# Kernel optimization log

Measured on AMD Instinct MI355X. Metric: run time of the kernel, lower is better.

The kernel has to match this reference:

```python
import math
import jax, jax.numpy as jnp
import numpy as np

N_HEAD = 16
N_GROUPS = 32
EPS = 1e-05


def gelu(x):
    return 0.5 * x * (1.0 + jnp.tanh(math.sqrt(2.0 / math.pi) * (x + 0.044715 * x ** 3)))


def dp_group_norm(x, weight, bias, num_groups=N_GROUPS, eps=EPS):
    # x: [B, T, H]. torch F.group_norm on transposed [B, H, T] normalizes over
    # (channels_per_group, T) jointly per (batch, group).
    B, T, H = x.shape
    xg = x.reshape(B, T, num_groups, H // num_groups)
    mean = jnp.mean(xg, axis=(1, 3), keepdims=True)
    var = jnp.mean((xg - mean) ** 2, axis=(1, 3), keepdims=True)
    xn = ((xg - mean) / jnp.sqrt(var + eps)).reshape(B, T, H)
    return xn * weight + bias


def attention(x, w_attn, b_attn, w_aproj, b_aproj):
    B, T, H = x.shape
    hd = H // N_HEAD
    qkv = x @ w_attn + b_attn                      # [B, T, 3H]
    q, k, v = jnp.split(qkv, 3, axis=-1)
    q = q.reshape(B, T, N_HEAD, hd).transpose(0, 2, 1, 3)   # [B, nh, T, hd]
    k = k.reshape(B, T, N_HEAD, hd).transpose(0, 2, 1, 3)   # [B, nh, T, hd]
    v = v.reshape(B, T, N_HEAD, hd).transpose(0, 2, 1, 3)
    w = jnp.einsum('bhqd,bhkd->bhqk', q, k)        # no 1/sqrt(d): scale=False
    causal = jnp.tril(jnp.ones((T, T), dtype=x.dtype))
    w = w * causal - 1e10 * (1.0 - causal)
    w = jax.nn.softmax(w, axis=-1)
    a = jnp.einsum('bhqk,bhkd->bhqd', w, v)        # [B, nh, T, hd]
    a = a.transpose(0, 2, 1, 3).reshape(B, T, H)
    a = a @ w_aproj + b_aproj
    present = jnp.stack((k, v))                    # [2, B, nh, T, hd]
    return a, present


def setup_inputs() -> dict:
    key = jax.random.key(0)
    ks = jax.random.split(key, 6)
    B, T, H = 2, 2048, 1024
    return {
        'x': jax.random.normal(ks[0], (B, T, H), dtype=jnp.float32),
        'w_attn': jax.random.normal(ks[1], (H, 3 * H), dtype=jnp.float32) * 0.02,
        'b_attn': jnp.zeros((3 * H,), dtype=jnp.float32),
        'w_aproj': jax.random.normal(ks[2], (H, H), dtype=jnp.float32) * 0.02,
        'b_aproj': jnp.zeros((H,), dtype=jnp.float32),
        'ln1_w': jnp.ones((H,), dtype=jnp.float32),
        'ln1_b': jnp.zeros((H,), dtype=jnp.float32),
        'ln2_w': jnp.ones((H,), dtype=jnp.float32),
        'ln2_b': jnp.zeros((H,), dtype=jnp.float32),
        'w_fc': jax.random.normal(ks[3], (H, 4 * H), dtype=jnp.float32) * 0.02,
        'b_fc': jnp.zeros((4 * H,), dtype=jnp.float32),
        'w_mproj': jax.random.normal(ks[4], (4 * H, H), dtype=jnp.float32) * 0.02,
        'b_mproj': jnp.zeros((H,), dtype=jnp.float32),
    }


def reference(x, w_attn, b_attn, w_aproj, b_aproj, ln1_w, ln1_b, ln2_w, ln2_b,
              w_fc, b_fc, w_mproj, b_mproj):
    a, present = attention(dp_group_norm(x, ln1_w, ln1_b), w_attn, b_attn, w_aproj, b_aproj)
    x = x + a
    h = gelu(dp_group_norm(x, ln2_w, ln2_b) @ w_fc + b_fc)
    m = h @ w_mproj + b_mproj
    x = x + m
    return (x, present)
```

## Files before the change

### kernel.cpp

```cpp
#include <hip/hip_runtime.h>

#define B_  2
#define T_  2048
#define H_  1024
#define NH_ 16
#define HD_ 64
#define M_  (B_*T_)
#define PS_ 72

typedef __bf16 bf16x8 __attribute__((ext_vector_type(8)));
typedef float  floatx4 __attribute__((ext_vector_type(4)));

typedef __attribute__((address_space(1))) const unsigned int gas_u32;
typedef __attribute__((address_space(3))) unsigned int       las_u32;

__device__ __forceinline__ void gload_lds16(const __bf16* g, __bf16* l) {
    __builtin_amdgcn_global_load_lds((gas_u32*)g, (las_u32*)l, 16, 0, 0);
}

__global__ __launch_bounds__(256) void transpose_bf16(
    const float* __restrict__ in, __bf16* __restrict__ out, int K, int N)
{
    __shared__ float tile[32][33];
    const int k0 = blockIdx.x * 32, n0 = blockIdx.y * 32;
    const int tx = threadIdx.x & 31, ty = threadIdx.x >> 5;
#pragma unroll
    for (int i = 0; i < 32; i += 8)
        tile[ty + i][tx] = in[(size_t)(k0 + ty + i) * N + (n0 + tx)];
    __syncthreads();
#pragma unroll
    for (int i = 0; i < 32; i += 8)
        out[(size_t)(n0 + ty + i) * K + (k0 + tx)] = (__bf16)tile[tx][ty + i];
}

__global__ __launch_bounds__(256) void gn_partial(
    const float* __restrict__ x, float2* __restrict__ part)
{
    const int bg = blockIdx.x, chunk = blockIdx.y;
    const int batch = bg >> 5, g = bg & 31;
    const float* xp = x + (size_t)batch * T_ * H_ + g * 32;
    float s = 0.f, ss = 0.f;
    for (int i = threadIdx.x; i < 128 * 32; i += 256) {
        const int t = chunk * 128 + (i >> 5), c = i & 31;
        const float v = xp[(size_t)t * H_ + c];
        s += v; ss += v * v;
    }
#pragma unroll
    for (int off = 32; off > 0; off >>= 1) {
        s  += __shfl_down(s,  off, 64);
        ss += __shfl_down(ss, off, 64);
    }
    __shared__ float rs[4], rss[4];
    const int wv = threadIdx.x >> 6, lane = threadIdx.x & 63;
    if (lane == 0) { rs[wv] = s; rss[wv] = ss; }
    __syncthreads();
    if (threadIdx.x == 0)
        part[bg * 16 + chunk] =
            make_float2(rs[0] + rs[1] + rs[2] + rs[3],
                        rss[0] + rss[1] + rss[2] + rss[3]);
}

__global__ __launch_bounds__(64) void gn_finalize(
    const float2* __restrict__ part, float2* __restrict__ stats)
{
    const int bg = threadIdx.x;
    float s = 0.f, ss = 0.f;
#pragma unroll
    for (int i = 0; i < 16; ++i) {
        const float2 p = part[bg * 16 + i];
        s += p.x; ss += p.y;
    }
    const float inv = 1.f / (float)(T_ * 32);
    const float mean = s * inv;
    const float var  = ss * inv - mean * mean;
    stats[bg] = make_float2(mean, rsqrtf(var + 1e-5f));
}

__global__ __launch_bounds__(256) void gn_apply(
    const float* __restrict__ x, const float2* __restrict__ stats,
    const float* __restrict__ w, const float* __restrict__ bsc,
    __bf16* __restrict__ out)
{
    const size_t idx = ((size_t)blockIdx.x * 256 + threadIdx.x) * 4;
    const int h = (int)(idx & (H_ - 1));
    const int batch = (int)(idx >> 21);
    const float2 mr = stats[batch * 32 + (h >> 5)];
    const float4 xv = *(const float4*)(x + idx);
    const float4 wv = *(const float4*)(w + h);
    const float4 bv = *(const float4*)(bsc + h);
    __bf16 o[4];
    o[0] = (__bf16)((xv.x - mr.x) * mr.y * wv.x + bv.x);
    o[1] = (__bf16)((xv.y - mr.x) * mr.y * wv.y + bv.y);
    o[2] = (__bf16)((xv.z - mr.x) * mr.y * wv.z + bv.z);
    o[3] = (__bf16)((xv.w - mr.x) * mr.y * wv.w + bv.w);
    *(uint2*)(out + idx) = *(uint2*)o;
}

__device__ __forceinline__ void gemm_core(
    const __bf16* __restrict__ A, const __bf16* __restrict__ BT,
    int K, int m0, int n0, __bf16* As, __bf16* Bs, floatx4 (&acc)[4][4])
{
    const int tid  = threadIdx.x;
    const int lane = tid & 63, wv = tid >> 6;
    const int quad = lane >> 4, l16 = lane & 15;
    const int wm = (wv >> 1) * 64, wn = (wv & 1) * 64;
    const int r0 = tid >> 2;
    const int scs = (((tid & 3) ^ ((r0 >> 1) & 3)) * 8);
    const int xq8 = (quad ^ ((l16 >> 1) & 3)) * 8;

    const __bf16* Ag = A  + (size_t)(m0 + r0) * K + scs;
    const __bf16* Bg = BT + (size_t)(n0 + r0) * K + scs;

#pragma unroll
    for (int s = 0; s < 2; ++s) {
        gload_lds16(Ag + s * 32,                  As + s * 4096 + tid * 8);
        gload_lds16(Ag + (size_t)64 * K + s * 32, As + s * 4096 + 2048 + tid * 8);
        gload_lds16(Bg + s * 32,                  Bs + s * 4096 + tid * 8);
        gload_lds16(Bg + (size_t)64 * K + s * 32, Bs + s * 4096 + 2048 + tid * 8);
    }
    int cur = 0;
    for (int kt = 0; kt < K; kt += 64) {
        if (kt + 64 < K) {
            const int nb = (cur ^ 1) * 8192;
            const int kn = kt + 64;
#pragma unroll
            for (int s = 0; s < 2; ++s) {
                gload_lds16(Ag + kn + s * 32,                  As + nb + s * 4096 + tid * 8);
                gload_lds16(Ag + (size_t)64 * K + kn + s * 32, As + nb + s * 4096 + 2048 + tid * 8);
                gload_lds16(Bg + kn + s * 32,                  Bs + nb + s * 4096 + tid * 8);
                gload_lds16(Bg + (size_t)64 * K + kn + s * 32, Bs + nb + s * 4096 + 2048 + tid * 8);
            }
            asm volatile("s_waitcnt vmcnt(8)" ::: "memory");
        } else {
            asm volatile("s_waitcnt vmcnt(0)" ::: "memory");
        }
        __builtin_amdgcn_s_barrier();
        __builtin_amdgcn_sched_barrier(0);
        const __bf16* Ab = As + cur * 8192;
        const __bf16* Bb = Bs + cur * 8192;
#pragma unroll
        for (int kk = 0; kk < 2; ++kk) {
            bf16x8 af[4], bfg[4];
#pragma unroll
            for (int i = 0; i < 4; ++i)
                af[i]  = *(const bf16x8*)(Ab + kk * 4096 + (wm + i * 16 + l16) * 32 + xq8);
#pragma unroll
            for (int i = 0; i < 4; ++i)
                bfg[i] = *(const bf16x8*)(Bb + kk * 4096 + (wn + i * 16 + l16) * 32 + xq8);
#pragma unroll
            for (int mi = 0; mi < 4; ++mi)
#pragma unroll
                for (int ni = 0; ni < 4; ++ni)
                    acc[mi][ni] = __builtin_amdgcn_mfma_f32_16x16x32_bf16(
                        af[mi], bfg[ni], acc[mi][ni], 0, 0, 0);
        }
        __builtin_amdgcn_sched_barrier(0);
        __builtin_amdgcn_s_barrier();
        __builtin_amdgcn_sched_barrier(0);
        cur ^= 1;
    }
}

#define GEMM_PROLOGUE(KVAL)                                             \
    __shared__ __align__(16) __bf16 As[2 * 8192], Bs[2 * 8192];         \
    const int m0 = blockIdx.x * 128, n0 = blockIdx.y * 128;             \
    floatx4 acc[4][4];                                                  \
    { floatx4 z = {0.f, 0.f, 0.f, 0.f};                                 \
      for (int i = 0; i < 4; ++i) for (int j = 0; j < 4; ++j) acc[i][j] = z; } \
    gemm_core(A, BT, (KVAL), m0, n0, As, Bs, acc);                      \
    const int tid = threadIdx.x, lane = tid & 63, wv = tid >> 6;        \
    const int quad = lane >> 4, l16 = lane & 15;                        \
    const int wm = (wv >> 1) * 64, wn = (wv & 1) * 64;                  \
    (void)tid;

__global__ __launch_bounds__(256) void gemm_qkv(
    const __bf16* __restrict__ A, const __bf16* __restrict__ BT,
    const float* __restrict__ bias, __bf16* __restrict__ qb,
    __bf16* __restrict__ kb, __bf16* __restrict__ vtb,
    float* __restrict__ present)
{
    GEMM_PROLOGUE(H_)
#pragma unroll
    for (int ni = 0; ni < 4; ++ni) {
        const int col = n0 + wn + ni * 16 + l16;
        const float bv = bias[col];
        const int which = col >> 10, c = col & 1023, hh = c >> 6, d = c & 63;
#pragma unroll
        for (int mi = 0; mi < 4; ++mi)
#pragma unroll
            for (int r = 0; r < 4; ++r) {
                const int row = m0 + wm + mi * 16 + quad * 4 + r;
                const int bb = row >> 11, t = row & 2047;
                const float v = acc[mi][ni][r] + bv;
                const size_t idx = (((size_t)bb * NH_ + hh) * T_ + t) * HD_ + d;
                if (which == 0)      qb[idx] = (__bf16)(v * 1.4426950408889634f);
                else if (which == 1) { kb[idx] = (__bf16)v; present[idx] = v; }
                else { vtb[(((size_t)bb * NH_ + hh) * HD_ + d) * T_ + t] = (__bf16)v;
                       present[(size_t)B_ * NH_ * T_ * HD_ + idx] = v; }
            }
    }
}

__global__ __launch_bounds__(256) void gemm_gelu(
    const __bf16* __restrict__ A, const __bf16* __restrict__ BT,
    const float* __restrict__ bias, __bf16* __restrict__ out)
{
    GEMM_PROLOGUE(H_)
#pragma unroll
    for (int ni = 0; ni < 4; ++ni) {
        const int col = n0 + wn + ni * 16 + l16;
        const float bv = bias[col];
#pragma unroll
        for (int mi = 0; mi < 4; ++mi)
#pragma unroll
            for (int r = 0; r < 4; ++r) {
                const int row = m0 + wm + mi * 16 + quad * 4 + r;
                const float v = acc[mi][ni][r] + bv;
                const float e = exp2f(-2.3022082f * (v + 0.044715f * v * v * v));
                float rcp;
                asm("v_rcp_f32 %0, %1" : "=v"(rcp) : "v"(1.f + e));
                out[(size_t)row * (4 * H_) + col] = (__bf16)(v * rcp);
            }
    }
}

__global__ __launch_bounds__(256) void gemm_resid_n64(
    const __bf16* __restrict__ A, const __bf16* __restrict__ BT,
    const float* __restrict__ bias, const float* __restrict__ resid,
    float* __restrict__ out, int K, int N)
{
    __shared__ __align__(16) __bf16 As[2 * 8192], Bs[2 * 4096];
    const int m0 = blockIdx.x * 128, n0 = blockIdx.y * 64;
    const int tid  = threadIdx.x;
    const int lane = tid & 63, wv = tid >> 6;
    const int quad = lane >> 4, l16 = lane & 15;
    const int wm = (wv >> 1) * 64, wn = (wv & 1) * 32;
    const int r0 = tid >> 2;
    const int scs = (((tid & 3) ^ ((r0 >> 1) & 3)) * 8);
    const int xq8 = (quad ^ ((l16 >> 1) & 3)) * 8;

    floatx4 acc[4][2];
    { floatx4 z = {0.f, 0.f, 0.f, 0.f};
#pragma unroll
      for (int i = 0; i < 4; ++i) { acc[i][0] = z; acc[i][1] = z; } }

    const __bf16* Ag = A  + (size_t)(m0 + r0) * K + scs;
    const __bf16* Bg = BT + (size_t)(n0 + r0) * K + scs;

#pragma unroll
    for (int s = 0; s < 2; ++s) {
        gload_lds16(Ag + s * 32,                  As + s * 4096 + tid * 8);
        gload_lds16(Ag + (size_t)64 * K + s * 32, As + s * 4096 + 2048 + tid * 8);
        gload_lds16(Bg + s * 32,                  Bs + s * 2048 + tid * 8);
    }
    int cur = 0;
    for (int kt = 0; kt < K; kt += 64) {
        if (kt + 64 < K) {
            const int kn = kt + 64;
            const int nbA = (cur ^ 1) * 8192, nbB = (cur ^ 1) * 4096;
#pragma unroll
            for (int s = 0; s < 2; ++s) {
                gload_lds16(Ag + kn + s * 32,                  As + nbA + s * 4096 + tid * 8);
                gload_lds16(Ag + (size_t)64 * K + kn + s * 32, As + nbA + s * 4096 + 2048 + tid * 8);
                gload_lds16(Bg + kn + s * 32,                  Bs + nbB + s * 2048 + tid * 8);
            }
            asm volatile("s_waitcnt vmcnt(6)" ::: "memory");
        } else {
            asm volatile("s_waitcnt vmcnt(0)" ::: "memory");
        }
        __builtin_amdgcn_s_barrier();
        __builtin_amdgcn_sched_barrier(0);
        const __bf16* Ab = As + cur * 8192;
        const __bf16* Bb = Bs + cur * 4096;
#pragma unroll
        for (int kk = 0; kk < 2; ++kk) {
            bf16x8 af[4], bfg[2];
#pragma unroll
            for (int i = 0; i < 4; ++i)
                af[i]  = *(const bf16x8*)(Ab + kk * 4096 + (wm + i * 16 + l16) * 32 + xq8);
#pragma unroll
            for (int i = 0; i < 2; ++i)
                bfg[i] = *(const bf16x8*)(Bb + kk * 2048 + (wn + i * 16 + l16) * 32 + xq8);
#pragma unroll
            for (int mi = 0; mi < 4; ++mi)
#pragma unroll
                for (int ni = 0; ni < 2; ++ni)
                    acc[mi][ni] = __builtin_amdgcn_mfma_f32_16x16x32_bf16(
                        af[mi], bfg[ni], acc[mi][ni], 0, 0, 0);
        }
        __builtin_amdgcn_sched_barrier(0);
        __builtin_amdgcn_s_barrier();
        __builtin_amdgcn_sched_barrier(0);
        cur ^= 1;
    }

#pragma unroll
    for (int ni = 0; ni < 2; ++ni) {
        const int col = n0 + wn + ni * 16 + l16;
        const float bv = bias[col];
#pragma unroll
        for (int mi = 0; mi < 4; ++mi)
#pragma unroll
            for (int r = 0; r < 4; ++r) {
                const int row = m0 + wm + mi * 16 + quad * 4 + r;
                const size_t idx = (size_t)row * N + col;
                out[idx] = acc[mi][ni][r] + bv + resid[idx];
            }
    }
}

__global__ __launch_bounds__(256) void attn_kernel(
    const __bf16* __restrict__ qb, const __bf16* __restrict__ kb,
    const __bf16* __restrict__ vtb, __bf16* __restrict__ aout)
{
    const int bh = blockIdx.x;
    const int sp = 31 - blockIdx.y;
    const int bb = bh >> 4, hh = bh & 15;
    const __bf16* Q  = qb  + (size_t)bh * T_ * HD_;
    const __bf16* Kp = kb  + (size_t)bh * T_ * HD_;
    const __bf16* VT = vtb + (size_t)bh * HD_ * T_;
    __shared__ __align__(16) __bf16 Qs[2 * 2048];
    __shared__ __align__(16) __bf16 Ks[2][2 * 2048];
    __shared__ __align__(16) __bf16 Vs[2][2 * 2048];
    __shared__ __align__(16) __bf16 Ps[64 * PS_];

    const int tid = threadIdx.x, lane = tid & 63, wv = tid >> 6;
    const int quad = lane >> 4, l16 = lane & 15;
    const int sr = tid >> 2;
    const int scs = (((tid & 3) ^ ((sr >> 1) & 3)) * 8);
    const int xq8 = (quad ^ ((l16 >> 1) & 3)) * 8;

    const int q0 = sp * 64, nkt = sp + 1;

#pragma unroll
    for (int s = 0; s < 2; ++s) {
        gload_lds16(Q  + (size_t)(q0 + sr) * HD_ + s * 32 + scs, Qs + s * 2048 + tid * 8);
        gload_lds16(Kp + (size_t)sr * HD_ + s * 32 + scs, &Ks[0][s * 2048 + tid * 8]);
        gload_lds16(VT + (size_t)sr * T_  + s * 32 + scs, &Vs[0][s * 2048 + tid * 8]);
    }
    asm volatile("s_waitcnt vmcnt(0)" ::: "memory");
    __builtin_amdgcn_s_barrier();
    __builtin_amdgcn_sched_barrier(0);

    bf16x8 aq[2];
#pragma unroll
    for (int kk = 0; kk < 2; ++kk)
        aq[kk] = *(const bf16x8*)(Qs + kk * 2048 + (wv * 16 + l16) * 32 + xq8);

    float m_i[4], l_p[4];
    floatx4 Ov[4];
    { floatx4 z = {0.f, 0.f, 0.f, 0.f};
#pragma unroll
      for (int i = 0; i < 4; ++i) { Ov[i] = z; m_i[i] = -1e30f; l_p[i] = 0.f; } }

    int cur = 0;
    for (int kt = 0; kt < nkt; ++kt) {
        if (kt + 1 < nkt) {
            const int kn = (kt + 1) * 64;
#pragma unroll
            for (int s = 0; s < 2; ++s) {
                gload_lds16(Kp + (size_t)(kn + sr) * HD_ + s * 32 + scs,
                            &Ks[cur ^ 1][s * 2048 + tid * 8]);
                gload_lds16(VT + (size_t)sr * T_ + kn + s * 32 + scs,
                            &Vs[cur ^ 1][s * 2048 + tid * 8]);
            }
            asm volatile("s_waitcnt vmcnt(4)" ::: "memory");
        } else {
            asm volatile("s_waitcnt vmcnt(0)" ::: "memory");
        }
        __builtin_amdgcn_s_barrier();
        __builtin_amdgcn_sched_barrier(0);

        const __bf16* Kc = Ks[cur];
        const __bf16* Vc = Vs[cur];

        floatx4 sacc[4];
        { floatx4 z = {0.f, 0.f, 0.f, 0.f};
#pragma unroll
          for (int i = 0; i < 4; ++i) sacc[i] = z; }
#pragma unroll
        for (int kk = 0; kk < 2; ++kk)
#pragma unroll
            for (int ni = 0; ni < 4; ++ni) {
                const bf16x8 bk = *(const bf16x8*)(Kc + kk * 2048 + (ni * 16 + l16) * 32 + xq8);
                sacc[ni] = __builtin_amdgcn_mfma_f32_16x16x32_bf16(aq[kk], bk, sacc[ni], 0, 0, 0);
            }
        if (kt == sp) {
#pragma unroll
            for (int ni = 0; ni < 4; ++ni) {
                const int keyL = ni * 16 + l16;
#pragma unroll
                for (int r = 0; r < 4; ++r)
                    if (keyL > quad * 4 + r + wv * 16) sacc[ni][r] = -1e30f;
            }
        }
        float rmax[4];
#pragma unroll
        for (int r = 0; r < 4; ++r)
            rmax[r] = fmaxf(fmaxf(sacc[0][r], sacc[1][r]),
                            fmaxf(sacc[2][r], sacc[3][r]));
#pragma unroll
        for (int off = 1; off < 16; off <<= 1)
#pragma unroll
            for (int r = 0; r < 4; ++r)
                rmax[r] = fmaxf(rmax[r], __shfl_xor(rmax[r], off, 64));
        float need = rmax[0] - m_i[0];
#pragma unroll
        for (int r = 1; r < 4; ++r) need = fmaxf(need, rmax[r] - m_i[r]);
        if (__any(need > 8.f)) {
#pragma unroll
            for (int r = 0; r < 4; ++r) {
                const float mn = fmaxf(m_i[r], rmax[r]);
                const float al = exp2f(m_i[r] - mn);
                m_i[r] = mn;
                l_p[r] *= al;
#pragma unroll
                for (int ni = 0; ni < 4; ++ni) Ov[ni][r] *= al;
            }
        }
#pragma unroll
        for (int ni = 0; ni < 4; ++ni)
#pragma unroll
            for (int r = 0; r < 4; ++r) {
                const float pe = exp2f(sacc[ni][r] - m_i[r]);
                sacc[ni][r] = pe;
                l_p[r] += pe;
            }
#pragma unroll
        for (int ni = 0; ni < 4; ++ni)
#pragma unroll
            for (int r = 0; r < 4; ++r)
                Ps[(wv * 16 + quad * 4 + r) * PS_ + ni * 16 + l16] = (__bf16)sacc[ni][r];
#pragma unroll
        for (int kk = 0; kk < 2; ++kk) {
            const bf16x8 ap = *(const bf16x8*)(Ps + (wv * 16 + l16) * PS_ + kk * 32 + quad * 8);
#pragma unroll
            for (int ni = 0; ni < 4; ++ni) {
                const bf16x8 bv2 = *(const bf16x8*)(Vc + kk * 2048 + (ni * 16 + l16) * 32 + xq8);
                Ov[ni] = __builtin_amdgcn_mfma_f32_16x16x32_bf16(ap, bv2, Ov[ni], 0, 0, 0);
            }
        }
        __builtin_amdgcn_sched_barrier(0);
        __builtin_amdgcn_s_barrier();
        __builtin_amdgcn_sched_barrier(0);
        cur ^= 1;
    }
#pragma unroll
    for (int off = 1; off < 16; off <<= 1)
#pragma unroll
        for (int r = 0; r < 4; ++r)
            l_p[r] += __shfl_xor(l_p[r], off, 64);
#pragma unroll
    for (int ni = 0; ni < 4; ++ni)
#pragma unroll
        for (int r = 0; r < 4; ++r) {
            const int t = q0 + wv * 16 + quad * 4 + r;
            aout[((size_t)(bb * T_ + t)) * H_ + hh * HD_ + ni * 16 + l16] =
                (__bf16)(Ov[ni][r] / l_p[r]);
        }
}

extern "C" void kernel_launch(void* const* d_in, const int* in_sizes, int n_in,
                              void* d_out, int out_size, void* d_ws, size_t ws_size,
                              hipStream_t stream)
{
    (void)in_sizes; (void)n_in; (void)out_size; (void)ws_size;
    const float* x       = (const float*)d_in[0];
    const float* w_attn  = (const float*)d_in[1];
    const float* b_attn  = (const float*)d_in[2];
    const float* w_aproj = (const float*)d_in[3];
    const float* b_aproj = (const float*)d_in[4];
    const float* ln1_w   = (const float*)d_in[5];
    const float* ln1_b   = (const float*)d_in[6];
    const float* ln2_w   = (const float*)d_in[7];
    const float* ln2_b   = (const float*)d_in[8];
    const float* w_fc    = (const float*)d_in[9];
    const float* b_fc    = (const float*)d_in[10];
    const float* w_mproj = (const float*)d_in[11];
    const float* b_mproj = (const float*)d_in[12];
    float* out = (float*)d_out;
    float* present = out + (size_t)M_ * H_;

    char* wp = (char*)d_ws;
    auto alloc = [&](size_t bytes) {
        void* p = (void*)wp; wp += (bytes + 255) & ~(size_t)255; return p;
    };
    __bf16* A1       = (__bf16*)alloc((size_t)M_ * H_ * 2);
    __bf16* A2       = (__bf16*)alloc((size_t)M_ * H_ * 2);
    __bf16* WattnT   = (__bf16*)alloc((size_t)3 * H_ * H_ * 2);
    __bf16* WaprojT  = (__bf16*)alloc((size_t)H_ * H_ * 2);
    __bf16* WfcT     = (__bf16*)alloc((size_t)4 * H_ * H_ * 2);
    __bf16* WmprojT  = (__bf16*)alloc((size_t)4 * H_ * H_ * 2);
    __bf16* qb       = (__bf16*)alloc((size_t)M_ * H_ * 2);
    __bf16* kb       = (__bf16*)alloc((size_t)M_ * H_ * 2);
    __bf16* vtb      = (__bf16*)alloc((size_t)M_ * H_ * 2);
    __bf16* attn_out = (__bf16*)alloc((size_t)M_ * H_ * 2);
    float*  x2       = (float*) alloc((size_t)M_ * H_ * 4);
    __bf16* Hbuf     = (__bf16*)alloc((size_t)M_ * 4 * H_ * 2);
    float2* gn_part  = (float2*)alloc(64 * 16 * sizeof(float2));
    float2* gn_stats = (float2*)alloc(64 * sizeof(float2));

    transpose_bf16<<<dim3(H_/32, 3*H_/32), 256, 0, stream>>>(w_attn,  WattnT,  H_,   3*H_);
    transpose_bf16<<<dim3(H_/32, H_/32),   256, 0, stream>>>(w_aproj, WaprojT, H_,   H_);
    transpose_bf16<<<dim3(H_/32, 4*H_/32), 256, 0, stream>>>(w_fc,    WfcT,    H_,   4*H_);
    transpose_bf16<<<dim3(4*H_/32, H_/32), 256, 0, stream>>>(w_mproj, WmprojT, 4*H_, H_);

    gn_partial <<<dim3(64, 16), 256, 0, stream>>>(x, gn_part);
    gn_finalize<<<1, 64, 0, stream>>>(gn_part, gn_stats);
    gn_apply   <<<M_*H_/1024, 256, 0, stream>>>(x, gn_stats, ln1_w, ln1_b, A1);

    gemm_qkv<<<dim3(M_/128, 3*H_/128), 256, 0, stream>>>(A1, WattnT, b_attn,
                                                         qb, kb, vtb, present);
    attn_kernel<<<dim3(32, 32), 256, 0, stream>>>(qb, kb, vtb, attn_out);
    gemm_resid_n64<<<dim3(M_/128, H_/64), 256, 0, stream>>>(attn_out, WaprojT, b_aproj,
                                                            x, x2, H_, H_);

    gn_partial <<<dim3(64, 16), 256, 0, stream>>>(x2, gn_part);
    gn_finalize<<<1, 64, 0, stream>>>(gn_part, gn_stats);
    gn_apply   <<<M_*H_/1024, 256, 0, stream>>>(x2, gn_stats, ln2_w, ln2_b, A2);

    gemm_gelu<<<dim3(M_/128, 4*H_/128), 256, 0, stream>>>(A2, WfcT, b_fc, Hbuf);
    gemm_resid_n64<<<dim3(M_/128, H_/64), 256, 0, stream>>>(Hbuf, WmprojT, b_mproj,
                                                            x2, out, 4*H_, H_);
}
```

Before: 409.9 us.

## Use 256x256 tiles with 512 threads and triple-buffered K pipeline for QKV/FC GEMMs

Replaces the 128x128 GEMM core used by the QKV and FC+GELU kernels with a 256x256 tile computed by 8 waves (512 threads). Each wave now owns a 128x64 sub-tile. The K loop steps by 32 through a three-stage LDS ring with prefetch distance two, and MFMA issue is bracketed with s_setprio. The intent is more data reuse per LDS load and better latency hiding. In exchange each thread holds twice as many accumulator registers, the block uses 96 KB of LDS, and the QKV grid drops to 192 blocks, which may leave compute units idle.

```diff
diff --git a/kernel.cpp b/kernel.cpp
--- a/kernel.cpp
+++ b/kernel.cpp
@@ -96,97 +96,92 @@
     *(uint2*)(out + idx) = *(uint2*)o;
 }
 
-__device__ __forceinline__ void gemm_core(
+__device__ __forceinline__ void gemm_core256(
     const __bf16* __restrict__ A, const __bf16* __restrict__ BT,
-    int K, int m0, int n0, __bf16* As, __bf16* Bs, floatx4 (&acc)[4][4])
-{
-    const int tid  = threadIdx.x;
-    const int lane = tid & 63, wv = tid >> 6;
+    int K, int m0, int n0, __bf16* Sb, floatx4 (&acc)[8][4])
+{
+    const int tid = threadIdx.x, lane = tid & 63, wid = tid >> 6;
     const int quad = lane >> 4, l16 = lane & 15;
-    const int wm = (wv >> 1) * 64, wn = (wv & 1) * 64;
-    const int r0 = tid >> 2;
-    const int scs = (((tid & 3) ^ ((r0 >> 1) & 3)) * 8);
+    const int wm = (wid >> 2) * 128, wn = (wid & 3) * 64;
+    const int r0 = tid >> 2, cbs = tid & 3;
+    const int sc  = ((cbs ^ ((r0 >> 1) & 3)) * 8);
     const int xq8 = (quad ^ ((l16 >> 1) & 3)) * 8;
 
-    const __bf16* Ag = A  + (size_t)(m0 + r0) * K + scs;
-    const __bf16* Bg = BT + (size_t)(n0 + r0) * K + scs;
-
-#pragma unroll
-    for (int s = 0; s < 2; ++s) {
-        gload_lds16(Ag + s * 32,                  As + s * 4096 + tid * 8);
-        gload_lds16(Ag + (size_t)64 * K + s * 32, As + s * 4096 + 2048 + tid * 8);
-        gload_lds16(Bg + s * 32,                  Bs + s * 4096 + tid * 8);
-        gload_lds16(Bg + (size_t)64 * K + s * 32, Bs + s * 4096 + 2048 + tid * 8);
-    }
+    const __bf16* Ag = A  + (size_t)(m0 + r0) * K + sc;
+    const __bf16* Bg = BT + (size_t)(n0 + r0) * K + sc;
+
+#define STG256(b, kt)  do {                                                   \
+    gload_lds16(Ag + (kt),                  Sb + ((b)*2+0)*8192 + tid*8);     \
+    gload_lds16(Ag + (size_t)128*K + (kt),  Sb + ((b)*2+0)*8192 + 4096 + tid*8); \
+    gload_lds16(Bg + (kt),                  Sb + ((b)*2+1)*8192 + tid*8);     \
+    gload_lds16(Bg + (size_t)128*K + (kt),  Sb + ((b)*2+1)*8192 + 4096 + tid*8); } while (0)
+
+    STG256(0, 0);
+    STG256(1, 32);
     int cur = 0;
-    for (int kt = 0; kt < K; kt += 64) {
+    for (int kt = 0; kt < K; kt += 32) {
         if (kt + 64 < K) {
-            const int nb = (cur ^ 1) * 8192;
-            const int kn = kt + 64;
-#pragma unroll
-            for (int s = 0; s < 2; ++s) {
-                gload_lds16(Ag + kn + s * 32,                  As + nb + s * 4096 + tid * 8);
-                gload_lds16(Ag + (size_t)64 * K + kn + s * 32, As + nb + s * 4096 + 2048 + tid * 8);
-                gload_lds16(Bg + kn + s * 32,                  Bs + nb + s * 4096 + tid * 8);
-                gload_lds16(Bg + (size_t)64 * K + kn + s * 32, Bs + nb + s * 4096 + 2048 + tid * 8);
-            }
+            int nb = cur + 2; if (nb >= 3) nb -= 3;
+            STG256(nb, kt + 64);
             asm volatile("s_waitcnt vmcnt(8)" ::: "memory");
+        } else if (kt + 32 < K) {
+            asm volatile("s_waitcnt vmcnt(4)" ::: "memory");
         } else {
             asm volatile("s_waitcnt vmcnt(0)" ::: "memory");
         }
         __builtin_amdgcn_s_barrier();
         __builtin_amdgcn_sched_barrier(0);
-        const __bf16* Ab = As + cur * 8192;
-        const __bf16* Bb = Bs + cur * 8192;
-#pragma unroll
-        for (int kk = 0; kk < 2; ++kk) {
-            bf16x8 af[4], bfg[4];
-#pragma unroll
-            for (int i = 0; i < 4; ++i)
-                af[i]  = *(const bf16x8*)(Ab + kk * 4096 + (wm + i * 16 + l16) * 32 + xq8);
-#pragma unroll
-            for (int i = 0; i < 4; ++i)
-                bfg[i] = *(const bf16x8*)(Bb + kk * 4096 + (wn + i * 16 + l16) * 32 + xq8);
-#pragma unroll
-            for (int mi = 0; mi < 4; ++mi)
-#pragma unroll
-                for (int ni = 0; ni < 4; ++ni)
-                    acc[mi][ni] = __builtin_amdgcn_mfma_f32_16x16x32_bf16(
-                        af[mi], bfg[ni], acc[mi][ni], 0, 0, 0);
-        }
+        const __bf16* Ab = Sb + (cur*2+0)*8192;
+        const __bf16* Bb = Sb + (cur*2+1)*8192;
+        bf16x8 af[8], bfg[4];
+#pragma unroll
+        for (int i = 0; i < 8; ++i)
+            af[i]  = *(const bf16x8*)(Ab + (wm + i * 16 + l16) * 32 + xq8);
+#pragma unroll
+        for (int i = 0; i < 4; ++i)
+            bfg[i] = *(const bf16x8*)(Bb + (wn + i * 16 + l16) * 32 + xq8);
+        __builtin_amdgcn_s_setprio(1);
+#pragma unroll
+        for (int mi = 0; mi < 8; ++mi)
+#pragma unroll
+            for (int ni = 0; ni < 4; ++ni)
+                acc[mi][ni] = __builtin_amdgcn_mfma_f32_16x16x32_bf16(
+                    af[mi], bfg[ni], acc[mi][ni], 0, 0, 0);
+        __builtin_amdgcn_s_setprio(0);
         __builtin_amdgcn_sched_barrier(0);
         __builtin_amdgcn_s_barrier();
         __builtin_amdgcn_sched_barrier(0);
-        cur ^= 1;
-    }
-}
-
-#define GEMM_PROLOGUE(KVAL)                                             \
-    __shared__ __align__(16) __bf16 As[2 * 8192], Bs[2 * 8192];         \
-    const int m0 = blockIdx.x * 128, n0 = blockIdx.y * 128;             \
-    floatx4 acc[4][4];                                                  \
+        cur = cur + 1; if (cur >= 3) cur = 0;
+    }
+#undef STG256
+}
+
+#define GEMM256_PROLOGUE(KVAL, NB0)                                     \
+    __shared__ __align__(16) __bf16 Sb[6 * 8192];            \
+    const int m0 = blockIdx.x * 256, n0 = blockIdx.y * 256;             \
+    floatx4 acc[8][4];                                                  \
     { floatx4 z = {0.f, 0.f, 0.f, 0.f};                                 \
-      for (int i = 0; i < 4; ++i) for (int j = 0; j < 4; ++j) acc[i][j] = z; } \
-    gemm_core(A, BT, (KVAL), m0, n0, As, Bs, acc);                      \
-    const int tid = threadIdx.x, lane = tid & 63, wv = tid >> 6;        \
+      for (int i = 0; i < 8; ++i) for (int j = 0; j < 4; ++j) acc[i][j] = z; } \
+    gemm_core256(A, BT, (KVAL), m0, n0, Sb, acc);                       \
+    const int tid = threadIdx.x, lane = tid & 63, wid = tid >> 6;       \
     const int quad = lane >> 4, l16 = lane & 15;                        \
-    const int wm = (wv >> 1) * 64, wn = (wv & 1) * 64;                  \
-    (void)tid;
-
-__global__ __launch_bounds__(256) void gemm_qkv(
+    const int wm = (wid >> 2) * 128, wn = (wid & 3) * 64;               \
+    (void)tid; (void)NB0;
+
+__global__ __launch_bounds__(512) void gemm_qkv(
     const __bf16* __restrict__ A, const __bf16* __restrict__ BT,
     const float* __restrict__ bias, __bf16* __restrict__ qb,
     __bf16* __restrict__ kb, __bf16* __restrict__ vtb,
     float* __restrict__ present)
 {
-    GEMM_PROLOGUE(H_)
+    GEMM256_PROLOGUE(H_, 0)
 #pragma unroll
     for (int ni = 0; ni < 4; ++ni) {
         const int col = n0 + wn + ni * 16 + l16;
         const float bv = bias[col];
         const int which = col >> 10, c = col & 1023, hh = c >> 6, d = c & 63;
 #pragma unroll
-        for (int mi = 0; mi < 4; ++mi)
+        for (int mi = 0; mi < 8; ++mi)
 #pragma unroll
             for (int r = 0; r < 4; ++r) {
                 const int row = m0 + wm + mi * 16 + quad * 4 + r;
@@ -201,17 +196,17 @@
     }
 }
 
-__global__ __launch_bounds__(256) void gemm_gelu(
+__global__ __launch_bounds__(512) void gemm_gelu(
     const __bf16* __restrict__ A, const __bf16* __restrict__ BT,
     const float* __restrict__ bias, __bf16* __restrict__ out)
 {
-    GEMM_PROLOGUE(H_)
+    GEMM256_PROLOGUE(H_, 0)
 #pragma unroll
     for (int ni = 0; ni < 4; ++ni) {
         const int col = n0 + wn + ni * 16 + l16;
         const float bv = bias[col];
 #pragma unroll
-        for (int mi = 0; mi < 4; ++mi)
+        for (int mi = 0; mi < 8; ++mi)
 #pragma unroll
             for (int r = 0; r < 4; ++r) {
                 const int row = m0 + wm + mi * 16 + quad * 4 + r;
@@ -509,7 +504,7 @@
     gn_finalize<<<1, 64, 0, stream>>>(gn_part, gn_stats);
     gn_apply   <<<M_*H_/1024, 256, 0, stream>>>(x, gn_stats, ln1_w, ln1_b, A1);
 
-    gemm_qkv<<<dim3(M_/128, 3*H_/128), 256, 0, stream>>>(A1, WattnT, b_attn,
+    gemm_qkv<<<dim3(M_/256, 3*H_/256), 512, 0, stream>>>(A1, WattnT, b_attn,
                                                          qb, kb, vtb, present);
     attn_kernel<<<dim3(32, 32), 256, 0, stream>>>(qb, kb, vtb, attn_out);
     gemm_resid_n64<<<dim3(M_/128, H_/64), 256, 0, stream>>>(attn_out, WaprojT, b_aproj,
@@ -519,7 +514,7 @@
     gn_finalize<<<1, 64, 0, stream>>>(gn_part, gn_stats);
     gn_apply   <<<M_*H_/1024, 256, 0, stream>>>(x2, gn_stats, ln2_w, ln2_b, A2);
 
-    gemm_gelu<<<dim3(M_/128, 4*H_/128), 256, 0, stream>>>(A2, WfcT, b_fc, Hbuf);
+    gemm_gelu<<<dim3(M_/256, 4*H_/256), 512, 0, stream>>>(A2, WfcT, b_fc, Hbuf);
     gemm_resid_n64<<<dim3(M_/128, H_/64), 256, 0, stream>>>(Hbuf, WmprojT, b_mproj,
                                                             x2, out, 4*H_, H_);
 }
```

After: 416.9 us. About the same (+1.7%).
